# Kernel tuning notes

Hardware: AMD Instinct MI355X
Metric: run time of the kernel (lower is better)

## Reference

```python
import jax, jax.numpy as jnp
import numpy as np

N_NODES = 100000
N_EDGES = 3200000
IN_FEATS = 128
OUT_FEATS = 16
NEG_SLOPE = 0.2


def setup_inputs() -> dict:
    key = jax.random.key(0)
    k1, k2, k3, k4, k5, k6 = jax.random.split(key, 6)
    h = jax.random.normal(k1, (N_NODES, IN_FEATS), dtype=jnp.float32)
    src = jax.random.randint(k2, (N_EDGES,), 0, N_NODES, dtype=jnp.int64)
    dst = jax.random.randint(k3, (N_EDGES,), 0, N_NODES, dtype=jnp.int64)
    W = jax.random.normal(k4, (OUT_FEATS, IN_FEATS), dtype=jnp.float32) * (1.0 / np.sqrt(IN_FEATS))
    a_l = jax.random.normal(k5, (1, OUT_FEATS), dtype=jnp.float32) * (1.0 / np.sqrt(OUT_FEATS))
    a_r = jax.random.normal(k6, (1, OUT_FEATS), dtype=jnp.float32) * (1.0 / np.sqrt(OUT_FEATS))
    return {"h": h, "src": src, "dst": dst, "W": W, "a_l": a_l, "a_r": a_r}


def reference(h, src, dst, W, a_l, a_r):
    N = h.shape[0]
    # node projection: h @ fc.weight.T  -> [N, out]
    hW = h @ W.T
    # per-node attention logits: [N, 1]
    el = hW @ a_l.T
    er = hW @ a_r.T
    # u_add_v: per-edge logit e = el[src] + er[dst], then leaky_relu(0.2)
    e = jax.nn.leaky_relu(el[src] + er[dst], negative_slope=NEG_SLOPE)  # [E, 1]
    # edge_softmax over edges grouped by destination node (numerically stable)
    emax = jax.ops.segment_max(e, dst, num_segments=N)  # [N, 1], -inf for empty
    emax = jnp.where(jnp.isfinite(emax), emax, 0.0)
    e_exp = jnp.exp(e - emax[dst])
    esum = jax.ops.segment_sum(e_exp, dst, num_segments=N)  # [N, 1]
    alpha = e_exp / jnp.maximum(esum[dst], 1e-16)  # [E, 1]
    # u_mul_e + sum: weighted aggregation of source features at destinations
    out = jax.ops.segment_sum(hW[src] * alpha, dst, num_segments=N)  # [N, out]
    return out
```

## Files before the change

### kernel.cpp

```cpp
#include <hip/hip_runtime.h>
#include <hip/hip_bf16.h>
#include <stdint.h>

#define IN_F 128
#define OUT_F 16
#define NEG_SLOPE 0.2f
#define LB_BITS 7
#define LB_NODES 128
#define NB 782
#define CAP 4608
#define SC_E 16384

#define OFF_WSUM 3128
#define OFF_PREF 3160
#define OFF_GBASE 4726
#define OFF_SORTP 6304
#define SMEM_BYTES (OFF_SORTP + SC_E * 4)

__device__ __forceinline__ float u2f(uint32_t u) {
  union { uint32_t i; float f; } c;
  c.i = u;
  return c.f;
}

__global__ __launch_bounds__(512) void proj_scatter_kernel(
    const float* __restrict__ h, const float* __restrict__ W,
    const float* __restrict__ a_l, const float* __restrict__ a_r,
    const int* __restrict__ src, const int* __restrict__ dst,
    __hip_bfloat16* __restrict__ hWbf, float* __restrict__ el,
    float* __restrict__ er, int* __restrict__ cursor,
    uint32_t* __restrict__ payload, int N, int E, int scatBlocks) {
  __shared__ __align__(16) uint8_t smem[SMEM_BYTES];
  int t = threadIdx.x;

  int bid = (int)blockIdx.x;
  bool isScat = (bid & 1) == 0 && (bid >> 1) < scatBlocks;
  int sbid = bid >> 1;
  int pbid = (bid & 1) ? (bid >> 1) : (bid >> 1);
  if ((bid & 1) == 0 && sbid >= scatBlocks) {
    isScat = false;
    pbid = sbid;
  }

  if (isScat) {
    int* hist = (int*)smem;
    int* wsum = (int*)(smem + OFF_WSUM);
    unsigned short* pref = (unsigned short*)(smem + OFF_PREF);
    unsigned short* gbase = (unsigned short*)(smem + OFF_GBASE);
    uint32_t* sortedP = (uint32_t*)(smem + OFF_SORTP);

    int start = sbid * SC_E;
    int end = min(E, start + SC_E);
    int cnt = end - start;
    int lane = t & 63, wv = t >> 6;

    for (int i = t; i < NB; i += 512) hist[i] = 0;
    __syncthreads();

    const int4* d4 = (const int4*)(dst + start);
    int n4 = cnt >> 2;
    for (int i = t; i < n4; i += 512) {
      int4 d = d4[i];
      atomicAdd(&hist[d.x >> LB_BITS], 1);
      atomicAdd(&hist[d.y >> LB_BITS], 1);
      atomicAdd(&hist[d.z >> LB_BITS], 1);
      atomicAdd(&hist[d.w >> LB_BITS], 1);
    }
    for (int i = start + (n4 << 2) + t; i < end; i += 512)
      atomicAdd(&hist[dst[i] >> LB_BITS], 1);
    __syncthreads();

    int b0 = t * 2;
    int c0 = (b0 < NB) ? hist[b0] : 0;
    int c1 = (b0 + 1 < NB) ? hist[b0 + 1] : 0;
    int s_loc = c0 + c1;
    int inc = s_loc;
#pragma unroll
    for (int off = 1; off < 64; off <<= 1) {
      int v = __shfl_up(inc, off, 64);
      if (lane >= off) inc += v;
    }
    if (lane == 63) wsum[wv] = inc;
    __syncthreads();
    int pre = inc - s_loc;
    for (int w = 0; w < wv; ++w) pre += wsum[w];
    if (b0 < NB) {
      pref[b0] = (unsigned short)pre;
      int g = c0 ? atomicAdd(&cursor[b0 * 16], c0) : 0;
      gbase[b0] = (unsigned short)min(g, CAP);
      hist[b0] = 0;
    }
    if (b0 + 1 < NB) {
      pref[b0 + 1] = (unsigned short)(pre + c0);
      int g = c1 ? atomicAdd(&cursor[(b0 + 1) * 16], c1) : 0;
      gbase[b0 + 1] = (unsigned short)min(g, CAP);
      hist[b0 + 1] = 0;
    }
    if (b0 < NB && b0 + 2 >= NB)
      pref[NB] = (unsigned short)(pre + s_loc);
    __syncthreads();

    const int4* s4 = (const int4*)(src + start);
    for (int i = t; i < n4; i += 512) {
      int4 d = d4[i];
      int4 s = s4[i];
#pragma unroll
      for (int j = 0; j < 4; ++j) {
        int dd = j == 0 ? d.x : j == 1 ? d.y : j == 2 ? d.z : d.w;
        int ss = j == 0 ? s.x : j == 1 ? s.y : j == 2 ? s.z : s.w;
        int b = dd >> LB_BITS;
        int r = atomicAdd(&hist[b], 1);
        sortedP[(int)pref[b] + r] =
            ((uint32_t)ss << LB_BITS) | (uint32_t)(dd & (LB_NODES - 1));
      }
    }
    for (int i = start + (n4 << 2) + t; i < end; i += 512) {
      int dd = dst[i];
      int b = dd >> LB_BITS;
      int r = atomicAdd(&hist[b], 1);
      sortedP[(int)pref[b] + r] =
          ((uint32_t)src[i] << LB_BITS) | (uint32_t)(dd & (LB_NODES - 1));
    }
    __syncthreads();

    int g16 = t >> 4, l16 = t & 15;
    for (int b = g16; b < NB; b += 32) {
      int p0 = pref[b];
      int c = (int)pref[b + 1] - p0;
      if (c == 0) continue;
      int gb = gbase[b];
      size_t g0 = (size_t)b * CAP + (size_t)gb;
      for (int j = l16; j < c; j += 16)
        if (gb + j < CAP) payload[g0 + j] = sortedP[p0 + j];
    }
  } else {
    float* Ws = (float*)smem;
    for (int i = t; i < OUT_F * IN_F; i += 512) Ws[i] = W[i];
    __syncthreads();

    int node = pbid * 512 + t;
    if (node >= N) return;

    const float4* hrow = (const float4*)(h + (size_t)node * IN_F);
    float acc[OUT_F];
#pragma unroll
    for (int f = 0; f < OUT_F; ++f) acc[f] = 0.f;

#pragma unroll 4
    for (int k = 0; k < IN_F / 4; ++k) {
      float4 hv = hrow[k];
#pragma unroll
      for (int f = 0; f < OUT_F; ++f) {
        float4 wv = ((const float4*)(Ws + f * IN_F))[k];
        acc[f] += hv.x * wv.x + hv.y * wv.y + hv.z * wv.z + hv.w * wv.w;
      }
    }

    union {
      unsigned short us[OUT_F];
      uint4 q[2];
    } pk;
#pragma unroll
    for (int f = 0; f < OUT_F; ++f) {
      __hip_bfloat16 b = __float2bfloat16(acc[f]);
      pk.us[f] = *reinterpret_cast<unsigned short*>(&b);
    }
    uint4* dstq = (uint4*)(hWbf + (size_t)node * OUT_F);
    dstq[0] = pk.q[0];
    dstq[1] = pk.q[1];

    float vl = 0.f, vr = 0.f;
#pragma unroll
    for (int f = 0; f < OUT_F; ++f) {
      vl += acc[f] * a_l[f];
      vr += acc[f] * a_r[f];
    }
    el[node] = vl;
    er[node] = vr;
  }
}

__global__ __launch_bounds__(512) void agg_kernel(
    const uint32_t* __restrict__ payload, const int* __restrict__ cursor,
    const __hip_bfloat16* __restrict__ hWbf, const float* __restrict__ el,
    const float* __restrict__ er, float* __restrict__ out, int N) {
  __shared__ __align__(16) uint2 pairs[CAP];
  __shared__ int hist[LB_NODES];
  __shared__ int pref[LB_NODES];
  __shared__ int rank[LB_NODES];
  __shared__ float erS[LB_NODES];

  int t = threadIdx.x;
  int b = blockIdx.x;
  size_t base = (size_t)b * CAP;
  int cnt = min(cursor[b * 16], CAP);
  int node0 = b << LB_BITS;

  if (t < LB_NODES) {
    hist[t] = 0;
    rank[t] = 0;
    int nd = node0 + t;
    erS[t] = nd < N ? er[nd] : 0.f;
  }
  __syncthreads();

  const uint4* pay4 = (const uint4*)(payload + base);
  int n4 = (cnt + 3) >> 2;
  for (int i = t; i < n4; i += 512) {
    uint4 v = pay4[i];
    int i0 = i << 2;
    if (i0 + 0 < cnt) atomicAdd(&hist[v.x & (LB_NODES - 1)], 1);
    if (i0 + 1 < cnt) atomicAdd(&hist[v.y & (LB_NODES - 1)], 1);
    if (i0 + 2 < cnt) atomicAdd(&hist[v.z & (LB_NODES - 1)], 1);
    if (i0 + 3 < cnt) atomicAdd(&hist[v.w & (LB_NODES - 1)], 1);
  }
  __syncthreads();

  if (t < LB_NODES) {
    int s = 0;
    for (int j = 0; j < t; ++j) s += hist[j];
    pref[t] = s;
  }
  __syncthreads();

  for (int i = t; i < cnt; i += 512) {
    uint32_t p = payload[base + i];
    int dl = (int)(p & (LB_NODES - 1));
    int r = atomicAdd(&rank[dl], 1);
    float x = el[p >> LB_BITS] + erS[dl];
    x = x > 0.f ? x : NEG_SLOPE * x;
    pairs[pref[dl] + r] = make_uint2(p, __float_as_uint(__expf(x)));
  }
  __syncthreads();

  int g = t >> 2;
  int f2 = t & 1;
  int sub = (t >> 1) & 1;
  int node = node0 + g;
  if (node < N) {
    int k0 = pref[g];
    int kend = k0 + hist[g];
    float a0 = 0, a1 = 0, a2 = 0, a3 = 0, a4 = 0, a5 = 0, a6 = 0, a7 = 0,
          es = 0;
    const uint4* hw4 = (const uint4*)hWbf;
#pragma unroll 4
    for (int k = k0 + sub; k < kend; k += 2) {
      uint2 q = pairs[k];
      float ex = __uint_as_float(q.y);
      uint4 w = hw4[(size_t)(q.x >> LB_BITS) * 2 + f2];
      a0 += ex * u2f(w.x << 16);
      a1 += ex * u2f(w.x & 0xffff0000u);
      a2 += ex * u2f(w.y << 16);
      a3 += ex * u2f(w.y & 0xffff0000u);
      a4 += ex * u2f(w.z << 16);
      a5 += ex * u2f(w.z & 0xffff0000u);
      a6 += ex * u2f(w.w << 16);
      a7 += ex * u2f(w.w & 0xffff0000u);
      es += ex;
    }
    a0 += __shfl_xor(a0, 2);
    a1 += __shfl_xor(a1, 2);
    a2 += __shfl_xor(a2, 2);
    a3 += __shfl_xor(a3, 2);
    a4 += __shfl_xor(a4, 2);
    a5 += __shfl_xor(a5, 2);
    a6 += __shfl_xor(a6, 2);
    a7 += __shfl_xor(a7, 2);
    es += __shfl_xor(es, 2);
    if (sub == 0) {
      float inv = 1.0f / fmaxf(es, 1e-16f);
      float4* op = (float4*)(out + (size_t)node * OUT_F + f2 * 8);
      op[0] = make_float4(a0 * inv, a1 * inv, a2 * inv, a3 * inv);
      op[1] = make_float4(a4 * inv, a5 * inv, a6 * inv, a7 * inv);
    }
  }
}

extern "C" void kernel_launch(void* const* d_in, const int* in_sizes, int n_in,
                              void* d_out, int out_size, void* d_ws, size_t ws_size,
                              hipStream_t stream) {
  const float* h   = (const float*)d_in[0];
  const int*   src = (const int*)d_in[1];
  const int*   dst = (const int*)d_in[2];
  const float* W   = (const float*)d_in[3];
  const float* a_l = (const float*)d_in[4];
  const float* a_r = (const float*)d_in[5];
  float* out = (float*)d_out;

  const int N = in_sizes[0] / IN_F;
  const int E = in_sizes[1];
  const int scatBlocks = (E + SC_E - 1) / SC_E;
  const int projBlocks = (N + 511) / 512;

  __hip_bfloat16* hWbf = (__hip_bfloat16*)d_ws;
  float* el = (float*)(hWbf + (size_t)N * OUT_F);
  float* er = el + N;
  int* cursor = (int*)(er + N);
  uint32_t* payload = (uint32_t*)(cursor + (size_t)NB * 16);

  hipMemsetAsync(cursor, 0, (size_t)NB * 16 * sizeof(int), stream);

  proj_scatter_kernel<<<scatBlocks + projBlocks, 512, 0, stream>>>(
      h, W, a_l, a_r, src, dst, hWbf, el, er, cursor, payload, N, E, scatBlocks);

  agg_kernel<<<NB, 512, 0, stream>>>(payload, cursor, hWbf, el, er, out, N);
}
```

Measured before the change: 171.9 us.

## Fuse scatter and projection roles into one block per CU

Replaces the interleaved grid of separate scatter blocks and projection blocks with a fixed 256-block grid. Each block first bins an even share of the edges, then projects an even share of the nodes. The aim is to balance work evenly across all CUs and shrink per-block shared memory. In exchange, each block now runs scatter and projection back to back instead of overlapping them across different blocks, and about a quarter of the threads sit idle during projection.

```diff
diff --git a/kernel.cpp b/kernel.cpp
--- a/kernel.cpp
+++ b/kernel.cpp
@@ -9,13 +9,15 @@
 #define LB_NODES 128
 #define NB 782
 #define CAP 4608
-#define SC_E 16384
+#define NBLK 256
+#define SC_MAX 12544
 
 #define OFF_WSUM 3128
 #define OFF_PREF 3160
 #define OFF_GBASE 4726
 #define OFF_SORTP 6304
-#define SMEM_BYTES (OFF_SORTP + SC_E * 4)
+#define OFF_WS 56480
+#define SMEM_BYTES (OFF_WS + 8192)
 
 __device__ __forceinline__ float u2f(uint32_t u) {
   union { uint32_t i; float f; } c;
@@ -29,28 +31,23 @@
     const int* __restrict__ src, const int* __restrict__ dst,
     __hip_bfloat16* __restrict__ hWbf, float* __restrict__ el,
     float* __restrict__ er, int* __restrict__ cursor,
-    uint32_t* __restrict__ payload, int N, int E, int scatBlocks) {
+    uint32_t* __restrict__ payload, int N, int E, int chunkE, int chunkN) {
   __shared__ __align__(16) uint8_t smem[SMEM_BYTES];
   int t = threadIdx.x;
-
   int bid = (int)blockIdx.x;
-  bool isScat = (bid & 1) == 0 && (bid >> 1) < scatBlocks;
-  int sbid = bid >> 1;
-  int pbid = (bid & 1) ? (bid >> 1) : (bid >> 1);
-  if ((bid & 1) == 0 && sbid >= scatBlocks) {
-    isScat = false;
-    pbid = sbid;
-  }
-
-  if (isScat) {
-    int* hist = (int*)smem;
-    int* wsum = (int*)(smem + OFF_WSUM);
-    unsigned short* pref = (unsigned short*)(smem + OFF_PREF);
-    unsigned short* gbase = (unsigned short*)(smem + OFF_GBASE);
-    uint32_t* sortedP = (uint32_t*)(smem + OFF_SORTP);
-
-    int start = sbid * SC_E;
-    int end = min(E, start + SC_E);
+
+  int* hist = (int*)smem;
+  int* wsum = (int*)(smem + OFF_WSUM);
+  unsigned short* pref = (unsigned short*)(smem + OFF_PREF);
+  unsigned short* gbase = (unsigned short*)(smem + OFF_GBASE);
+  uint32_t* sortedP = (uint32_t*)(smem + OFF_SORTP);
+  float* Ws = (float*)(smem + OFF_WS);
+
+  for (int i = t; i < OUT_F * IN_F; i += 512) Ws[i] = W[i];
+
+  {
+    int start = bid * chunkE;
+    int end = min(E, start + chunkE);
     int cnt = end - start;
     int lane = t & 63, wv = t >> 6;
 
@@ -133,50 +130,49 @@
       for (int j = l16; j < c; j += 16)
         if (gb + j < CAP) payload[g0 + j] = sortedP[p0 + j];
     }
-  } else {
-    float* Ws = (float*)smem;
-    for (int i = t; i < OUT_F * IN_F; i += 512) Ws[i] = W[i];
-    __syncthreads();
-
-    int node = pbid * 512 + t;
-    if (node >= N) return;
-
-    const float4* hrow = (const float4*)(h + (size_t)node * IN_F);
-    float acc[OUT_F];
-#pragma unroll
-    for (int f = 0; f < OUT_F; ++f) acc[f] = 0.f;
+  }
+
+  {
+    int node = bid * chunkN + t;
+    int nend = min(N, bid * chunkN + chunkN);
+    if (t < chunkN && node < nend) {
+      const float4* hrow = (const float4*)(h + (size_t)node * IN_F);
+      float acc[OUT_F];
+#pragma unroll
+      for (int f = 0; f < OUT_F; ++f) acc[f] = 0.f;
 
 #pragma unroll 4
-    for (int k = 0; k < IN_F / 4; ++k) {
-      float4 hv = hrow[k];
+      for (int k = 0; k < IN_F / 4; ++k) {
+        float4 hv = hrow[k];
+#pragma unroll
+        for (int f = 0; f < OUT_F; ++f) {
+          float4 wv = ((const float4*)(Ws + f * IN_F))[k];
+          acc[f] += hv.x * wv.x + hv.y * wv.y + hv.z * wv.z + hv.w * wv.w;
+        }
+      }
+
+      union {
+        unsigned short us[OUT_F];
+        uint4 q[2];
+      } pk;
 #pragma unroll
       for (int f = 0; f < OUT_F; ++f) {
-        float4 wv = ((const float4*)(Ws + f * IN_F))[k];
-        acc[f] += hv.x * wv.x + hv.y * wv.y + hv.z * wv.z + hv.w * wv.w;
+        __hip_bfloat16 b = __float2bfloat16(acc[f]);
+        pk.us[f] = *reinterpret_cast<unsigned short*>(&b);
       }
-    }
-
-    union {
-      unsigned short us[OUT_F];
-      uint4 q[2];
-    } pk;
-#pragma unroll
-    for (int f = 0; f < OUT_F; ++f) {
-      __hip_bfloat16 b = __float2bfloat16(acc[f]);
-      pk.us[f] = *reinterpret_cast<unsigned short*>(&b);
-    }
-    uint4* dstq = (uint4*)(hWbf + (size_t)node * OUT_F);
-    dstq[0] = pk.q[0];
-    dstq[1] = pk.q[1];
-
-    float vl = 0.f, vr = 0.f;
-#pragma unroll
-    for (int f = 0; f < OUT_F; ++f) {
-      vl += acc[f] * a_l[f];
-      vr += acc[f] * a_r[f];
-    }
-    el[node] = vl;
-    er[node] = vr;
+      uint4* dstq = (uint4*)(hWbf + (size_t)node * OUT_F);
+      dstq[0] = pk.q[0];
+      dstq[1] = pk.q[1];
+
+      float vl = 0.f, vr = 0.f;
+#pragma unroll
+      for (int f = 0; f < OUT_F; ++f) {
+        vl += acc[f] * a_l[f];
+        vr += acc[f] * a_r[f];
+      }
+      el[node] = vl;
+      er[node] = vr;
+    }
   }
 }
 
@@ -289,8 +285,8 @@
 
   const int N = in_sizes[0] / IN_F;
   const int E = in_sizes[1];
-  const int scatBlocks = (E + SC_E - 1) / SC_E;
-  const int projBlocks = (N + 511) / 512;
+  int chunkE = ((E + NBLK - 1) / NBLK + 3) & ~3;
+  int chunkN = (N + NBLK - 1) / NBLK;
 
   __hip_bfloat16* hWbf = (__hip_bfloat16*)d_ws;
   float* el = (float*)(hWbf + (size_t)N * OUT_F);
@@ -300,8 +296,9 @@
 
   hipMemsetAsync(cursor, 0, (size_t)NB * 16 * sizeof(int), stream);
 
-  proj_scatter_kernel<<<scatBlocks + projBlocks, 512, 0, stream>>>(
-      h, W, a_l, a_r, src, dst, hWbf, el, er, cursor, payload, N, E, scatBlocks);
+  proj_scatter_kernel<<<NBLK, 512, 0, stream>>>(
+      h, W, a_l, a_r, src, dst, hWbf, el, er, cursor, payload, N, E, chunkE,
+      chunkN);
 
   agg_kernel<<<NB, 512, 0, stream>>>(payload, cursor, hWbf, el, er, out, N);
 }
```

Measured after the change: 175.5 us. +2.1%, slower.
